# Kernel optimization log

Measured on AMD Instinct MI355X. Metric: run time of the kernel, lower is better.

Reference implementation:

```python
import jax, jax.numpy as jnp
import numpy as np
from math import sqrt

B, S, D, H = 4, 2048, 1024, 16
HD = D // H


def setup_inputs() -> dict:
    key = jax.random.key(0)
    ks = jax.random.split(key, 16)
    w = 0.02
    q = jax.random.normal(ks[0], (B, S, D), jnp.float32)
    k = jax.random.normal(ks[1], (B, S, D), jnp.float32)
    v = jax.random.normal(ks[2], (B, S, D), jnp.float32)
    # causal attention mask [1,1,S,S]
    attn_mask = jnp.tril(jnp.ones((S, S), jnp.int32))[None, None]
    # padding mask [B,1,1,S]; force position 0 valid so no softmax row is all -inf
    pad_mask = jax.random.randint(ks[3], (B, 1, 1, S), 0, 2, jnp.int32)
    pad_mask = pad_mask.at[..., 0].set(1)
    params = {
        'Wq': jax.random.normal(ks[4], (D, D), jnp.float32) * w,
        'bq': jnp.zeros((D,), jnp.float32),
        'Wk': jax.random.normal(ks[5], (D, D), jnp.float32) * w,
        'bk': jnp.zeros((D,), jnp.float32),
        'Wv': jax.random.normal(ks[6], (D, D), jnp.float32) * w,
        'bv': jnp.zeros((D,), jnp.float32),
        'Wo': jax.random.normal(ks[7], (D, D), jnp.float32) * w,
        'bo': jnp.zeros((D,), jnp.float32),
        'gamma': jnp.ones((D,), jnp.float32),
        'beta': jnp.zeros((D,), jnp.float32),
    }
    return dict(q=q, k=k, v=v, attn_mask=attn_mask, pad_mask=pad_mask, **params)


def _mha(q, k, v, Wq, bq, Wk, bk, Wv, bv, Wo, bo, gamma, beta, attn_mask, pad_mask):
    seq = q.shape[1]
    # residual path is detached in the original (q.clone().detach())
    x = jax.lax.stop_gradient(q)
    # Linear projections (torch Linear: y = x @ W.T + b)
    qp = (q @ Wq.T + bq).reshape(-1, H, seq, HD)   # raw view, NO head transpose (faithful)
    kp = (k @ Wk.T + bk).reshape(-1, H, seq, HD)
    vp = (v @ Wv.T + bv).reshape(-1, H, seq, HD)
    scores = jnp.einsum('bhqd,bhkd->bhqk', qp, kp)   # [B,H,S,S]
    scores = jnp.where(pad_mask == 0, -jnp.inf, scores)
    scores = jnp.where(attn_mask == 0, -jnp.inf, scores)
    # scaling applied AFTER masking, as in source
    attn = jax.nn.softmax(scores / sqrt(HD), axis=-1)
    out = jnp.einsum('bhqk,bhkd->bhqd', attn, vp).reshape(-1, seq, D)
    out = out @ Wo.T + bo  # dropout is identity in eval
    y = x + out
    mean = jnp.mean(y, axis=-1, keepdims=True)
    std = jnp.sqrt(jnp.mean((y - mean) ** 2, axis=-1, keepdims=True))
    return gamma * ((y - mean) / (std + 1e-8)) + beta


def reference(q, k, v, attn_mask, pad_mask, Wq, bq, Wk, bk, Wv, bv, Wo, bo, gamma, beta):
    return _mha(q, k, v, Wq, bq, Wk, bk, Wv, bv, Wo, bo, gamma, beta, attn_mask, pad_mask)
```

## Files before the change

### kernel.cpp

```cpp
#include <hip/hip_runtime.h>
#include <hip/hip_bf16.h>
#include <math.h>

#define B_  4
#define S_  2048
#define D_  1024
#define H_  16
#define HD_ 64
#define SD_  (S_*D_)
#define SHD_ (S_*HD_)

typedef __attribute__((ext_vector_type(8))) short          bf16x8;
typedef __attribute__((ext_vector_type(4))) float          f32x4;
typedef __attribute__((ext_vector_type(8))) unsigned short us8;
typedef __attribute__((ext_vector_type(4))) unsigned short us4;

__device__ __forceinline__ unsigned short f2bf(float x) {
  unsigned int u = __float_as_uint(x);
  u += 0x7fffu + ((u >> 16) & 1u);
  return (unsigned short)(u >> 16);
}
__device__ __forceinline__ float bf2f(unsigned short u) {
  return __uint_as_float(((unsigned int)u) << 16);
}

__device__ __forceinline__ void gload16(const unsigned short* g, unsigned short* l) {
  __builtin_amdgcn_global_load_lds(
      (const __attribute__((address_space(1))) unsigned int*)g,
      (__attribute__((address_space(3))) unsigned int*)l,
      16, 0, 0);
}

__device__ __forceinline__ void stage_swz(const unsigned short* __restrict__ g,
                                          int rstride ,
                                          unsigned short* lds, int tid)
{
#pragma unroll
  for (int rr = 0; rr < 2; ++rr) {
    const int cidx = tid + rr * 256;
    const int row  = cidx >> 3;
    const int sb   = ((cidx & 7) * 16) ^ ((row & 7) << 4);
    gload16(g + (size_t)row * rstride + (sb >> 1), lds + cidx * 8);
  }
}

__device__ __forceinline__ void read_frag_pair(const unsigned short* lds, int row,
                                               int quad, bf16x8& f0, bf16x8& f1)
{
  const int sw = (row & 7) << 4;
  const unsigned short* p = lds + row * 64;
  f0 = *(const bf16x8*)(p + (((quad * 16) ^ sw) >> 1));
  f1 = *(const bf16x8*)(p + (((64 + quad * 16) ^ sw) >> 1));
}

__global__ __launch_bounds__(256) void cvt_a(const float* __restrict__ s,
                                             unsigned short* __restrict__ d)
{
  int i = blockIdx.x * 256 + threadIdx.x;
  float4 v = ((const float4*)s)[i];
  us4 o = { f2bf(v.x), f2bf(v.y), f2bf(v.z), f2bf(v.w) };
  *(us4*)(d + (size_t)i * 4) = o;
}

__global__ __launch_bounds__(256) void cvt_w(const float* __restrict__ w0,
                                             const float* __restrict__ w1,
                                             const float* __restrict__ w2,
                                             const float* __restrict__ w3,
                                             unsigned short* __restrict__ dst)
{
  const float* s = (blockIdx.y == 0) ? w0 : (blockIdx.y == 1) ? w1
                 : (blockIdx.y == 2) ? w2 : w3;
  unsigned short* d = dst + (size_t)blockIdx.y * 1024 * 1024;
  int i = blockIdx.x * 256 + threadIdx.x;
  float4 v = ((const float4*)s)[i];
  us4 o = { f2bf(v.x), f2bf(v.y), f2bf(v.z), f2bf(v.w) };
  *(us4*)(d + (size_t)i * 4) = o;
}

__global__ __launch_bounds__(256) void gemm_mfma(
    const unsigned short* __restrict__ A,
    const unsigned short* __restrict__ Wb,
    const float* __restrict__ bias,
    unsigned short* __restrict__ Cb)
{
  __shared__ unsigned short As[128 * 32];
  __shared__ unsigned short Bs[128 * 32];

  const int tid  = threadIdx.x;
  const int lane = tid & 63;
  const int w    = tid >> 6;
  const int wm   = w >> 1, wn = w & 1;
  const int l16  = lane & 15, quad = lane >> 4;
  const int n0 = blockIdx.x * 128;
  const int m0 = blockIdx.y * 128;

  f32x4 acc[4][4];
#pragma unroll
  for (int mt = 0; mt < 4; ++mt)
#pragma unroll
    for (int nt = 0; nt < 4; ++nt) acc[mt][nt] = (f32x4){0.f, 0.f, 0.f, 0.f};

  const int srow = lane >> 2;
  const int sseg = (lane & 3) * 8;

  for (int kt = 0; kt < 32; ++kt) {
    const int kofs = kt * 32;
#pragma unroll
    for (int t = 0; t < 2; ++t) {
      const int r = w * 32 + t * 16 + srow;
      gload16(A  + (size_t)(m0 + r) * 1024 + kofs + sseg, &As[r * 32 + sseg]);
      gload16(Wb + (size_t)(n0 + r) * 1024 + kofs + sseg, &Bs[r * 32 + sseg]);
    }
    __syncthreads();

    bf16x8 af[4], bfr[4];
#pragma unroll
    for (int mt = 0; mt < 4; ++mt)
      af[mt] = *(const bf16x8*)&As[(wm * 64 + mt * 16 + l16) * 32 + quad * 8];
#pragma unroll
    for (int nt = 0; nt < 4; ++nt)
      bfr[nt] = *(const bf16x8*)&Bs[(wn * 64 + nt * 16 + l16) * 32 + quad * 8];
#pragma unroll
    for (int mt = 0; mt < 4; ++mt)
#pragma unroll
      for (int nt = 0; nt < 4; ++nt)
        acc[mt][nt] = __builtin_amdgcn_mfma_f32_16x16x32_bf16(
            af[mt], bfr[nt], acc[mt][nt], 0, 0, 0);
    __syncthreads();
  }

#pragma unroll
  for (int nt = 0; nt < 4; ++nt) {
    const int ncol = n0 + wn * 64 + nt * 16 + l16;
    const float bv = bias[ncol];
#pragma unroll
    for (int mt = 0; mt < 4; ++mt) {
      const int row = m0 + wm * 64 + mt * 16 + quad * 4;
#pragma unroll
      for (int reg = 0; reg < 4; ++reg)
        Cb[(size_t)(row + reg) * 1024 + ncol] = f2bf(acc[mt][nt][reg] + bv);
    }
  }
}

__global__ __launch_bounds__(256) void vtrans(
    const unsigned short* __restrict__ V, unsigned short* __restrict__ Vt)
{
  __shared__ unsigned short t[64][72];
  const int tid = threadIdx.x;
  const int st  = blockIdx.x;
  const int bh  = blockIdx.y;
  const unsigned short* src = V + (size_t)bh * SHD_ + (size_t)st * 4096;

#pragma unroll
  for (int u = tid; u < 512; u += 256) {
    us8 vv = ((const us8*)src)[u];
    int s  = u >> 3;
    int dg = (u & 7) * 8;
    *(us8*)&t[s][dg] = vv;
  }
  __syncthreads();

  unsigned short* dst = Vt + (size_t)bh * SHD_ + st * 64;
#pragma unroll
  for (int u = tid; u < 1024; u += 256) {
    int d  = u >> 4;
    int s4 = (u & 15) * 4;
    us4 o = { t[s4][d], t[s4 + 1][d], t[s4 + 2][d], t[s4 + 3][d] };
    *(us4*)(dst + (size_t)d * 2048 + s4) = o;
  }
}

__global__ __launch_bounds__(256, 4) void attn_mfma(
    unsigned short* __restrict__ Qb, const unsigned short* __restrict__ Kb,
    const unsigned short* __restrict__ Vt, const int* __restrict__ pad)
{
  __shared__ unsigned short Ks[64 * 64];
  __shared__ unsigned short Vs[2][64 * 64];
  __shared__ unsigned short Ps[4][16][72];

  const int tid  = threadIdx.x;
  const int lane = tid & 63;
  const int w    = tid >> 6;
  const int p    = blockIdx.x;
  const int bh   = blockIdx.y;
  const int b    = bh >> 4;
  const size_t base = (size_t)bh * SHD_;

  const int l16  = lane & 15;
  const int quad = lane >> 4;

  for (int half = 0; half < 2; ++half) {
    const int it = half ? (31 - p) : p;

    bf16x8 qfrag[2];
    {
      const unsigned short* qrow = Qb + base + (size_t)(it * 64 + w * 16 + l16) * 64;
      qfrag[0] = *(const bf16x8*)(qrow + quad * 8);
      qfrag[1] = *(const bf16x8*)(qrow + 32 + quad * 8);
    }

    f32x4 oacc[4];
#pragma unroll
    for (int dt = 0; dt < 4; ++dt) oacc[dt] = (f32x4){0.f, 0.f, 0.f, 0.f};
    float mrow[4], lrow[4];
#pragma unroll
    for (int r = 0; r < 4; ++r) { mrow[r] = -INFINITY; lrow[r] = 0.f; }

    __syncthreads();
    stage_swz(Kb + base, 64, Ks, tid);
    stage_swz(Vt + base, 2048, Vs[0], tid);
    int padv[4];
#pragma unroll
    for (int ct = 0; ct < 4; ++ct) padv[ct] = pad[b * S_ + ct * 16 + l16];
    int cur = 0;

    for (int jt = 0; jt <= it; ++jt) {
      __syncthreads();

      f32x4 sacc[4];
#pragma unroll
      for (int ct = 0; ct < 4; ++ct) {
        bf16x8 k0, k1;
        read_frag_pair(Ks, ct * 16 + l16, quad, k0, k1);
        f32x4 s = (f32x4){0.f, 0.f, 0.f, 0.f};
        s = __builtin_amdgcn_mfma_f32_16x16x32_bf16(qfrag[0], k0, s, 0, 0, 0);
        s = __builtin_amdgcn_mfma_f32_16x16x32_bf16(qfrag[1], k1, s, 0, 0, 0);
        sacc[ct] = s;
      }

      int padn[4];
      if (jt < it) {
        __syncthreads();
        stage_swz(Kb + base + (size_t)(jt + 1) * 4096, 64, Ks, tid);
        stage_swz(Vt + base + (jt + 1) * 64, 2048, Vs[cur ^ 1], tid);
#pragma unroll
        for (int ct = 0; ct < 4; ++ct)
          padn[ct] = pad[b * S_ + (jt + 1) * 64 + ct * 16 + l16];
      }

      const int grow0 = it * 64 + w * 16 + quad * 4;
      float alpha[4];
#pragma unroll
      for (int reg = 0; reg < 4; ++reg) {
        const int gi = grow0 + reg;
        float lg[4];
        float mx = -INFINITY;
#pragma unroll
        for (int ct = 0; ct < 4; ++ct) {
          int gj = jt * 64 + ct * 16 + l16;
          bool ok = (gj <= gi) && (padv[ct] != 0);
          lg[ct] = ok ? sacc[ct][reg] * 0.125f : -INFINITY;
          mx = fmaxf(mx, lg[ct]);
        }
#pragma unroll
        for (int off = 1; off < 16; off <<= 1) mx = fmaxf(mx, __shfl_xor(mx, off, 64));
        float mnew = fmaxf(mrow[reg], mx);
        float a    = __expf(mrow[reg] - mnew);
        float sm   = 0.f;
#pragma unroll
        for (int ct = 0; ct < 4; ++ct) {
          float pe = __expf(lg[ct] - mnew);
          sm += pe;
          Ps[w][quad * 4 + reg][ct * 16 + l16] = f2bf(pe);
        }
#pragma unroll
        for (int off = 1; off < 16; off <<= 1) sm += __shfl_xor(sm, off, 64);
        lrow[reg]  = lrow[reg] * a + sm;
        mrow[reg]  = mnew;
        alpha[reg] = a;
      }
#pragma unroll
      for (int dt = 0; dt < 4; ++dt)
#pragma unroll
        for (int reg = 0; reg < 4; ++reg) oacc[dt][reg] *= alpha[reg];

      bf16x8 pfrag0 = *(const bf16x8*)&Ps[w][l16][quad * 8];
      bf16x8 pfrag1 = *(const bf16x8*)&Ps[w][l16][32 + quad * 8];

#pragma unroll
      for (int dt = 0; dt < 4; ++dt) {
        bf16x8 v0, v1;
        read_frag_pair(Vs[cur], dt * 16 + l16, quad, v0, v1);
        oacc[dt] = __builtin_amdgcn_mfma_f32_16x16x32_bf16(pfrag0, v0, oacc[dt], 0, 0, 0);
        oacc[dt] = __builtin_amdgcn_mfma_f32_16x16x32_bf16(pfrag1, v1, oacc[dt], 0, 0, 0);
      }

      if (jt < it) {
#pragma unroll
        for (int ct = 0; ct < 4; ++ct) padv[ct] = padn[ct];
        cur ^= 1;
      }
    }

#pragma unroll
    for (int reg = 0; reg < 4; ++reg) {
      const float rl = 1.0f / lrow[reg];
      unsigned short* orow = Qb + base + (size_t)(it * 64 + w * 16 + quad * 4 + reg) * 64;
#pragma unroll
      for (int dt = 0; dt < 4; ++dt)
        orow[dt * 16 + l16] = f2bf(oacc[dt][reg] * rl);
    }
  }
}

__global__ __launch_bounds__(256) void ln_kernel(
    const float* __restrict__ x, const unsigned short* __restrict__ O,
    const float* __restrict__ gamma, const float* __restrict__ beta,
    float* __restrict__ out)
{
  __shared__ float red[8];
  const int row = blockIdx.x;
  const int tid = threadIdx.x;
  float4 xv = ((const float4*)x)[(size_t)row * 256 + tid];
  us4 ov4 = *(const us4*)(O + (size_t)row * 1024 + tid * 4);
  float4 y = make_float4(xv.x + bf2f(ov4[0]), xv.y + bf2f(ov4[1]),
                         xv.z + bf2f(ov4[2]), xv.w + bf2f(ov4[3]));
  float s1 = y.x + y.y + y.z + y.w;
  float s2 = y.x*y.x + y.y*y.y + y.z*y.z + y.w*y.w;
#pragma unroll
  for (int off = 32; off >= 1; off >>= 1) {
    s1 += __shfl_xor(s1, off, 64);
    s2 += __shfl_xor(s2, off, 64);
  }
  if ((tid & 63) == 0) { red[tid >> 6] = s1; red[4 + (tid >> 6)] = s2; }
  __syncthreads();
  s1 = red[0] + red[1] + red[2] + red[3];
  s2 = red[4] + red[5] + red[6] + red[7];
  const float mean = s1 * (1.0f / 1024.0f);
  const float var  = fmaxf(s2 * (1.0f / 1024.0f) - mean * mean, 0.f);
  const float rstd = 1.0f / (sqrtf(var) + 1e-8f);
  float4 gv = ((const float4*)gamma)[tid];
  float4 bv = ((const float4*)beta)[tid];
  float4 r;
  r.x = gv.x * (y.x - mean) * rstd + bv.x;
  r.y = gv.y * (y.y - mean) * rstd + bv.y;
  r.z = gv.z * (y.z - mean) * rstd + bv.z;
  r.w = gv.w * (y.w - mean) * rstd + bv.w;
  ((float4*)out)[(size_t)row * 256 + tid] = r;
}

extern "C" void kernel_launch(void* const* d_in, const int* in_sizes, int n_in,
                              void* d_out, int out_size, void* d_ws, size_t ws_size,
                              hipStream_t stream)
{
  const float* q  = (const float*)d_in[0];
  const float* k  = (const float*)d_in[1];
  const float* v  = (const float*)d_in[2];
  const int*   pad = (const int*)d_in[4];
  const float* Wq = (const float*)d_in[5];
  const float* bq = (const float*)d_in[6];
  const float* Wk = (const float*)d_in[7];
  const float* bk = (const float*)d_in[8];
  const float* Wv = (const float*)d_in[9];
  const float* bv = (const float*)d_in[10];
  const float* Wo = (const float*)d_in[11];
  const float* bo = (const float*)d_in[12];
  const float* gamma = (const float*)d_in[13];
  const float* beta  = (const float*)d_in[14];
  float* out = (float*)d_out;

  char* ws = (char*)d_ws;
  const size_t MB = 1024 * 1024;
  unsigned short* Ac   = (unsigned short*)(ws);
  unsigned short* Qb   = (unsigned short*)(ws + 16 * MB);
  unsigned short* Kb   = (unsigned short*)(ws + 32 * MB);
  unsigned short* Vb   = (unsigned short*)(ws + 48 * MB);
  unsigned short* Vtb  = (unsigned short*)(ws + 64 * MB);
  unsigned short* Wall = (unsigned short*)(ws + 80 * MB);
  unsigned short* Obuf = Ac;

  dim3 gg(8, 64), bb(256);
  cvt_w<<<dim3(1024, 4), 256, 0, stream>>>(Wq, Wk, Wv, Wo, Wall);

  cvt_a<<<8192, 256, 0, stream>>>(q, Ac);
  gemm_mfma<<<gg, bb, 0, stream>>>(Ac, Wall + 0 * MB, bq, Qb);
  cvt_a<<<8192, 256, 0, stream>>>(k, Ac);
  gemm_mfma<<<gg, bb, 0, stream>>>(Ac, Wall + 1 * MB, bk, Kb);
  cvt_a<<<8192, 256, 0, stream>>>(v, Ac);
  gemm_mfma<<<gg, bb, 0, stream>>>(Ac, Wall + 2 * MB, bv, Vb);
  vtrans<<<dim3(32, 64), 256, 0, stream>>>(Vb, Vtb);

  attn_mfma<<<dim3(16, 64), 256, 0, stream>>>(Qb, Kb, Vtb, pad);

  gemm_mfma<<<gg, bb, 0, stream>>>(Qb, Wall + 3 * MB, bo, Obuf);
  ln_kernel<<<dim3(B_ * S_), 256, 0, stream>>>(q, Obuf, gamma, beta, out);
}
```

Baseline: 432.7 us.

## Batch QKV projections into one launch and transpose score MFMA for cheaper softmax

Merges the three input conversions and three QKV GEMMs into single 3D-grid launches when the workspace is large enough, which cuts launch count and lets the GPU fill with more blocks. In attention, the score MFMA operands are swapped so each lane holds one query row, replacing per-row 16-lane shuffle reductions with two cross-quad shuffles and enabling vectorized P writes to LDS. The padding mask is precomputed as an additive float bias and the causal mask is applied only on the diagonal tile. The larger workspace path needs 121 MB, and the new single-row-per-lane layout needs extra shuffles to broadcast rescale factors.

```diff
diff --git a/kernel.cpp b/kernel.cpp
--- a/kernel.cpp
+++ b/kernel.cpp
@@ -62,6 +62,19 @@
   *(us4*)(d + (size_t)i * 4) = o;
 }
 
+__global__ __launch_bounds__(256) void cvt3(const float* __restrict__ q,
+                                            const float* __restrict__ k,
+                                            const float* __restrict__ v,
+                                            unsigned short* __restrict__ dst)
+{
+  const float* s = (blockIdx.y == 0) ? q : (blockIdx.y == 1) ? k : v;
+  unsigned short* d = dst + (size_t)blockIdx.y * (B_ * (size_t)SD_);
+  int i = blockIdx.x * 256 + threadIdx.x;
+  float4 x = ((const float4*)s)[i];
+  us4 o = { f2bf(x.x), f2bf(x.y), f2bf(x.z), f2bf(x.w) };
+  *(us4*)(d + (size_t)i * 4) = o;
+}
+
 __global__ __launch_bounds__(256) void cvt_w(const float* __restrict__ w0,
                                              const float* __restrict__ w1,
                                              const float* __restrict__ w2,
@@ -77,11 +90,22 @@
   *(us4*)(d + (size_t)i * 4) = o;
 }
 
-__global__ __launch_bounds__(256) void gemm_mfma(
+__global__ __launch_bounds__(256) void pad_cvt(const int* __restrict__ pad,
+                                               float* __restrict__ padf)
+{
+  int i = (blockIdx.x * 256 + threadIdx.x) * 4;
+  int4 pv = *(const int4*)(pad + i);
+  float4 o = { pv.x ? 0.f : -1e30f, pv.y ? 0.f : -1e30f,
+               pv.z ? 0.f : -1e30f, pv.w ? 0.f : -1e30f };
+  *(float4*)(padf + i) = o;
+}
+
+__device__ __forceinline__ void gemm_body(
     const unsigned short* __restrict__ A,
     const unsigned short* __restrict__ Wb,
     const float* __restrict__ bias,
-    unsigned short* __restrict__ Cb)
+    unsigned short* __restrict__ Cb,
+    int n0, int m0)
 {
   __shared__ unsigned short As[128 * 32];
   __shared__ unsigned short Bs[128 * 32];
@@ -91,8 +115,6 @@
   const int w    = tid >> 6;
   const int wm   = w >> 1, wn = w & 1;
   const int l16  = lane & 15, quad = lane >> 4;
-  const int n0 = blockIdx.x * 128;
-  const int m0 = blockIdx.y * 128;
 
   f32x4 acc[4][4];
 #pragma unroll
@@ -143,6 +165,29 @@
   }
 }
 
+__global__ __launch_bounds__(256) void gemm_mfma(
+    const unsigned short* __restrict__ A, const unsigned short* __restrict__ Wb,
+    const float* __restrict__ bias, unsigned short* __restrict__ Cb)
+{
+  gemm_body(A, Wb, bias, Cb, blockIdx.x * 128, blockIdx.y * 128);
+}
+
+__global__ __launch_bounds__(256) void gemm_qkv(
+    const unsigned short* __restrict__ A3,
+    const unsigned short* __restrict__ Wall,
+    const float* __restrict__ bq, const float* __restrict__ bk,
+    const float* __restrict__ bv,
+    unsigned short* __restrict__ Qb, unsigned short* __restrict__ Kb,
+    unsigned short* __restrict__ Vb)
+{
+  const int z = blockIdx.z;
+  const unsigned short* A  = A3 + (size_t)z * (B_ * (size_t)SD_);
+  const unsigned short* Wb = Wall + (size_t)z * 1024 * 1024;
+  const float* bias = (z == 0) ? bq : (z == 1) ? bk : bv;
+  unsigned short* Cb = (z == 0) ? Qb : (z == 1) ? Kb : Vb;
+  gemm_body(A, Wb, bias, Cb, blockIdx.x * 128, blockIdx.y * 128);
+}
+
 __global__ __launch_bounds__(256) void vtrans(
     const unsigned short* __restrict__ V, unsigned short* __restrict__ Vt)
 {
@@ -173,7 +218,7 @@
 
 __global__ __launch_bounds__(256, 4) void attn_mfma(
     unsigned short* __restrict__ Qb, const unsigned short* __restrict__ Kb,
-    const unsigned short* __restrict__ Vt, const int* __restrict__ pad)
+    const unsigned short* __restrict__ Vt, const float* __restrict__ padf)
 {
   __shared__ unsigned short Ks[64 * 64];
   __shared__ unsigned short Vs[2][64 * 64];
@@ -203,16 +248,15 @@
     f32x4 oacc[4];
 #pragma unroll
     for (int dt = 0; dt < 4; ++dt) oacc[dt] = (f32x4){0.f, 0.f, 0.f, 0.f};
-    float mrow[4], lrow[4];
-#pragma unroll
-    for (int r = 0; r < 4; ++r) { mrow[r] = -INFINITY; lrow[r] = 0.f; }
+    float mS = -INFINITY, lS = 0.f;
 
     __syncthreads();
     stage_swz(Kb + base, 64, Ks, tid);
     stage_swz(Vt + base, 2048, Vs[0], tid);
-    int padv[4];
-#pragma unroll
-    for (int ct = 0; ct < 4; ++ct) padv[ct] = pad[b * S_ + ct * 16 + l16];
+    float4 pf[4];
+#pragma unroll
+    for (int ct = 0; ct < 4; ++ct)
+      pf[ct] = *(const float4*)(padf + b * S_ + ct * 16 + quad * 4);
     int cur = 0;
 
     for (int jt = 0; jt <= it; ++jt) {
@@ -224,60 +268,66 @@
         bf16x8 k0, k1;
         read_frag_pair(Ks, ct * 16 + l16, quad, k0, k1);
         f32x4 s = (f32x4){0.f, 0.f, 0.f, 0.f};
-        s = __builtin_amdgcn_mfma_f32_16x16x32_bf16(qfrag[0], k0, s, 0, 0, 0);
-        s = __builtin_amdgcn_mfma_f32_16x16x32_bf16(qfrag[1], k1, s, 0, 0, 0);
+        s = __builtin_amdgcn_mfma_f32_16x16x32_bf16(k0, qfrag[0], s, 0, 0, 0);
+        s = __builtin_amdgcn_mfma_f32_16x16x32_bf16(k1, qfrag[1], s, 0, 0, 0);
         sacc[ct] = s;
       }
 
-      int padn[4];
+      float4 pfn[4];
       if (jt < it) {
         __syncthreads();
         stage_swz(Kb + base + (size_t)(jt + 1) * 4096, 64, Ks, tid);
         stage_swz(Vt + base + (jt + 1) * 64, 2048, Vs[cur ^ 1], tid);
 #pragma unroll
         for (int ct = 0; ct < 4; ++ct)
-          padn[ct] = pad[b * S_ + (jt + 1) * 64 + ct * 16 + l16];
+          pfn[ct] = *(const float4*)(padf + b * S_ + (jt + 1) * 64 + ct * 16 + quad * 4);
       }
 
-      const int grow0 = it * 64 + w * 16 + quad * 4;
-      float alpha[4];
-#pragma unroll
-      for (int reg = 0; reg < 4; ++reg) {
-        const int gi = grow0 + reg;
-        float lg[4];
-        float mx = -INFINITY;
-#pragma unroll
-        for (int ct = 0; ct < 4; ++ct) {
-          int gj = jt * 64 + ct * 16 + l16;
-          bool ok = (gj <= gi) && (padv[ct] != 0);
-          lg[ct] = ok ? sacc[ct][reg] * 0.125f : -INFINITY;
-          mx = fmaxf(mx, lg[ct]);
+      float lg[4][4];
+      float mx = -INFINITY;
+#pragma unroll
+      for (int ct = 0; ct < 4; ++ct)
+#pragma unroll
+        for (int reg = 0; reg < 4; ++reg) {
+          float sc = fmaf(sacc[ct][reg], 0.125f, ((const float*)&pf[ct])[reg]);
+          if (jt == it) {
+            bool ok = (ct * 16 + quad * 4 + reg) <= (w * 16 + l16);
+            sc = ok ? sc : -1e30f;
+          }
+          lg[ct][reg] = sc;
+          mx = fmaxf(mx, sc);
         }
-#pragma unroll
-        for (int off = 1; off < 16; off <<= 1) mx = fmaxf(mx, __shfl_xor(mx, off, 64));
-        float mnew = fmaxf(mrow[reg], mx);
-        float a    = __expf(mrow[reg] - mnew);
-        float sm   = 0.f;
-#pragma unroll
-        for (int ct = 0; ct < 4; ++ct) {
-          float pe = __expf(lg[ct] - mnew);
+      mx = fmaxf(mx, __shfl_xor(mx, 16, 64));
+      mx = fmaxf(mx, __shfl_xor(mx, 32, 64));
+      const float mnew = fmaxf(mS, mx);
+      const float a    = __expf(mS - mnew);
+      float sm = 0.f;
+#pragma unroll
+      for (int ct = 0; ct < 4; ++ct) {
+        us4 pk;
+#pragma unroll
+        for (int reg = 0; reg < 4; ++reg) {
+          float pe = __expf(lg[ct][reg] - mnew);
           sm += pe;
-          Ps[w][quad * 4 + reg][ct * 16 + l16] = f2bf(pe);
+          pk[reg] = f2bf(pe);
         }
-#pragma unroll
-        for (int off = 1; off < 16; off <<= 1) sm += __shfl_xor(sm, off, 64);
-        lrow[reg]  = lrow[reg] * a + sm;
-        mrow[reg]  = mnew;
-        alpha[reg] = a;
+        *(us4*)&Ps[w][l16][ct * 16 + quad * 4] = pk;
       }
+      sm += __shfl_xor(sm, 16, 64);
+      sm += __shfl_xor(sm, 32, 64);
+      lS = lS * a + sm;
+      mS = mnew;
+
+      float aO[4];
+#pragma unroll
+      for (int reg = 0; reg < 4; ++reg) aO[reg] = __shfl(a, quad * 4 + reg, 64);
 #pragma unroll
       for (int dt = 0; dt < 4; ++dt)
 #pragma unroll
-        for (int reg = 0; reg < 4; ++reg) oacc[dt][reg] *= alpha[reg];
+        for (int reg = 0; reg < 4; ++reg) oacc[dt][reg] *= aO[reg];
 
       bf16x8 pfrag0 = *(const bf16x8*)&Ps[w][l16][quad * 8];
       bf16x8 pfrag1 = *(const bf16x8*)&Ps[w][l16][32 + quad * 8];
-
 #pragma unroll
       for (int dt = 0; dt < 4; ++dt) {
         bf16x8 v0, v1;
@@ -288,14 +338,17 @@
 
       if (jt < it) {
 #pragma unroll
-        for (int ct = 0; ct < 4; ++ct) padv[ct] = padn[ct];
+        for (int ct = 0; ct < 4; ++ct) pf[ct] = pfn[ct];
         cur ^= 1;
       }
     }
 
+    float lO[4];
+#pragma unroll
+    for (int reg = 0; reg < 4; ++reg) lO[reg] = __shfl(lS, quad * 4 + reg, 64);
 #pragma unroll
     for (int reg = 0; reg < 4; ++reg) {
-      const float rl = 1.0f / lrow[reg];
+      const float rl = 1.0f / lO[reg];
       unsigned short* orow = Qb + base + (size_t)(it * 64 + w * 16 + quad * 4 + reg) * 64;
 #pragma unroll
       for (int dt = 0; dt < 4; ++dt)
@@ -362,27 +415,47 @@
 
   char* ws = (char*)d_ws;
   const size_t MB = 1024 * 1024;
-  unsigned short* Ac   = (unsigned short*)(ws);
-  unsigned short* Qb   = (unsigned short*)(ws + 16 * MB);
-  unsigned short* Kb   = (unsigned short*)(ws + 32 * MB);
-  unsigned short* Vb   = (unsigned short*)(ws + 48 * MB);
-  unsigned short* Vtb  = (unsigned short*)(ws + 64 * MB);
-  unsigned short* Wall = (unsigned short*)(ws + 80 * MB);
-  unsigned short* Obuf = Ac;
-
   dim3 gg(8, 64), bb(256);
-  cvt_w<<<dim3(1024, 4), 256, 0, stream>>>(Wq, Wk, Wv, Wo, Wall);
-
-  cvt_a<<<8192, 256, 0, stream>>>(q, Ac);
-  gemm_mfma<<<gg, bb, 0, stream>>>(Ac, Wall + 0 * MB, bq, Qb);
-  cvt_a<<<8192, 256, 0, stream>>>(k, Ac);
-  gemm_mfma<<<gg, bb, 0, stream>>>(Ac, Wall + 1 * MB, bk, Kb);
-  cvt_a<<<8192, 256, 0, stream>>>(v, Ac);
-  gemm_mfma<<<gg, bb, 0, stream>>>(Ac, Wall + 2 * MB, bv, Vb);
-  vtrans<<<dim3(32, 64), 256, 0, stream>>>(Vb, Vtb);
-
-  attn_mfma<<<dim3(16, 64), 256, 0, stream>>>(Qb, Kb, Vtb, pad);
-
-  gemm_mfma<<<gg, bb, 0, stream>>>(Qb, Wall + 3 * MB, bo, Obuf);
-  ln_kernel<<<dim3(B_ * S_), 256, 0, stream>>>(q, Obuf, gamma, beta, out);
-}
+
+  if (ws_size >= 121 * MB) {
+    unsigned short* Ac3  = (unsigned short*)(ws);
+    unsigned short* Qb   = (unsigned short*)(ws + 48 * MB);
+    unsigned short* Kb   = (unsigned short*)(ws + 64 * MB);
+    unsigned short* Vb   = (unsigned short*)(ws + 80 * MB);
+    unsigned short* Vtb  = (unsigned short*)(ws + 96 * MB);
+    unsigned short* Wall = (unsigned short*)(ws + 112 * MB);
+    float*          padf = (float*)(ws + 120 * MB);
+    unsigned short* Obuf = Ac3;
+
+    cvt_w<<<dim3(1024, 4), 256, 0, stream>>>(Wq, Wk, Wv, Wo, Wall);
+    pad_cvt<<<8, 256, 0, stream>>>(pad, padf);
+    cvt3<<<dim3(8192, 3), 256, 0, stream>>>(q, k, v, Ac3);
+    gemm_qkv<<<dim3(8, 64, 3), bb, 0, stream>>>(Ac3, Wall, bq, bk, bv, Qb, Kb, Vb);
+    vtrans<<<dim3(32, 64), 256, 0, stream>>>(Vb, Vtb);
+    attn_mfma<<<dim3(16, 64), 256, 0, stream>>>(Qb, Kb, Vtb, padf);
+    gemm_mfma<<<gg, bb, 0, stream>>>(Qb, Wall + 3 * MB, bo, Obuf);
+    ln_kernel<<<dim3(B_ * S_), 256, 0, stream>>>(q, Obuf, gamma, beta, out);
+  } else {
+    unsigned short* Ac   = (unsigned short*)(ws);
+    unsigned short* Qb   = (unsigned short*)(ws + 16 * MB);
+    unsigned short* Kb   = (unsigned short*)(ws + 32 * MB);
+    unsigned short* Vb   = (unsigned short*)(ws + 48 * MB);
+    unsigned short* Vtb  = (unsigned short*)(ws + 64 * MB);
+    unsigned short* Wall = (unsigned short*)(ws + 80 * MB);
+    float*          padf = (float*)(ws + 88 * MB);
+    unsigned short* Obuf = Ac;
+
+    cvt_w<<<dim3(1024, 4), 256, 0, stream>>>(Wq, Wk, Wv, Wo, Wall);
+    pad_cvt<<<8, 256, 0, stream>>>(pad, padf);
+    cvt_a<<<8192, 256, 0, stream>>>(q, Ac);
+    gemm_mfma<<<gg, bb, 0, stream>>>(Ac, Wall + 0 * MB, bq, Qb);
+    cvt_a<<<8192, 256, 0, stream>>>(k, Ac);
+    gemm_mfma<<<gg, bb, 0, stream>>>(Ac, Wall + 1 * MB, bk, Kb);
+    cvt_a<<<8192, 256, 0, stream>>>(v, Ac);
+    gemm_mfma<<<gg, bb, 0, stream>>>(Ac, Wall + 2 * MB, bv, Vb);
+    vtrans<<<dim3(32, 64), 256, 0, stream>>>(Vb, Vtb);
+    attn_mfma<<<dim3(16, 64), 256, 0, stream>>>(Qb, Kb, Vtb, padf);
+    gemm_mfma<<<gg, bb, 0, stream>>>(Qb, Wall + 3 * MB, bo, Obuf);
+    ln_kernel<<<dim3(B_ * S_), 256, 0, stream>>>(q, Obuf, gamma, beta, out);
+  }
+}
```

After: 388.8 us. -10.1%, faster.
